# Kernel tuning notes

Measured on AMD Instinct MI355X. Metric: run time of the kernel, lower is better.

Reference implementation:

```python
import jax, jax.numpy as jnp
from jax import lax
import numpy as np

N, L, E, NHEAD, DFF = 16, 1024, 512, 8, 2048
HD = E // NHEAD
NLEVELS = 10  # log2(1024)
S_SCALES = NLEVELS + 1


def setup_inputs() -> dict:
    key = jax.random.key(0)
    ks = jax.random.split(key, 12)
    s = 0.05
    return {
        "src": jax.random.normal(ks[0], (N, L, E), jnp.float32),
        "conv_w": jax.random.normal(ks[1], (NLEVELS, HD, HD, 2), jnp.float32) * s,
        "conv_b": jax.random.normal(ks[2], (NLEVELS, HD), jnp.float32) * s,
        "in_proj_w": jax.random.normal(ks[3], (3 * E, E), jnp.float32) * s,
        "in_proj_b": jax.random.normal(ks[4], (3 * E,), jnp.float32) * s,
        "out_proj_w": jax.random.normal(ks[5], (E, E), jnp.float32) * s,
        "out_proj_b": jax.random.normal(ks[6], (E,), jnp.float32) * s,
        "ln1_w": jnp.ones((E,), jnp.float32),
        "ln1_b": jnp.zeros((E,), jnp.float32),
        "ln2_w": jnp.ones((E,), jnp.float32),
        "ln2_b": jnp.zeros((E,), jnp.float32),
        "w1": jax.random.normal(ks[7], (DFF, E), jnp.float32) * s,
        "b1": jax.random.normal(ks[8], (DFF,), jnp.float32) * s,
        "w2": jax.random.normal(ks[9], (E, DFF), jnp.float32) * s,
        "b2": jax.random.normal(ks[10], (E,), jnp.float32) * s,
    }


def _layer_norm(x, w, b, eps=1e-5):
    mu = jnp.mean(x, axis=-1, keepdims=True)
    var = jnp.mean(jnp.square(x - mu), axis=-1, keepdims=True)
    return (x - mu) * lax.rsqrt(var + eps) * w + b


def _forward(src, conv_w, conv_b, in_proj_w, in_proj_b, out_proj_w, out_proj_b,
             ln1_w, ln1_b, ln2_w, ln2_b, w1, b1, w2, b2):
    n, l, e = src.shape
    hd = e // NHEAD
    # pyramid over 1D spatial dim, channels-first
    out = jnp.transpose(src, (0, 2, 1))  # (N, E, L)
    hidden_vals = [out]
    for i in range(NLEVELS):
        x = out.reshape(n * NHEAD, hd, out.shape[-1])  # (N*H, hd, li)
        x = lax.conv_general_dilated(
            x, conv_w[i], window_strides=(2,), padding='VALID',
            dimension_numbers=('NCH', 'OIH', 'NCH'))
        x = jax.nn.relu(x + conv_b[i][None, :, None])
        out = x.reshape(n, e, x.shape[-1])  # (N, E, li/2)
        # upsample back to full length via repeat_interleave
        hidden_vals.append(jnp.repeat(out, l // out.shape[-1], axis=2))
    hv = jnp.stack(hidden_vals, -1)                      # (N, E, L, S)
    s = hv.shape[-1]
    hv = jnp.transpose(hv, (3, 0, 2, 1)).reshape(s, n * l, e)  # (S, N*L, E)

    # multi-head attention: length-1 query (finest scale) over all scales
    b_ = n * l
    q = hv[0:1] @ in_proj_w[:e].T + in_proj_b[:e]            # (1, B, E)
    k = hv @ in_proj_w[e:2 * e].T + in_proj_b[e:2 * e]       # (S, B, E)
    v = hv @ in_proj_w[2 * e:].T + in_proj_b[2 * e:]         # (S, B, E)
    qh = jnp.transpose(q.reshape(1, b_, NHEAD, hd), (1, 2, 0, 3))  # (B, H, 1, hd)
    kh = jnp.transpose(k.reshape(s, b_, NHEAD, hd), (1, 2, 0, 3))  # (B, H, S, hd)
    vh = jnp.transpose(v.reshape(s, b_, NHEAD, hd), (1, 2, 0, 3))  # (B, H, S, hd)
    scores = jnp.einsum('bhqd,bhkd->bhqk', qh, kh) / jnp.sqrt(jnp.float32(hd))
    attn = jax.nn.softmax(scores, axis=-1)
    o = jnp.einsum('bhqk,bhkd->bhqd', attn, vh)              # (B, H, 1, hd)
    o = o.reshape(b_, e) @ out_proj_w.T + out_proj_b         # (B, E)
    src2 = o.reshape(n, l, e)

    # faithful to source: residual computed then overwritten by norm1(src2)
    x = _layer_norm(src2, ln1_w, ln1_b)
    ff = jax.nn.relu(x @ w1.T + b1) @ w2.T + b2
    return _layer_norm(x + ff, ln2_w, ln2_b)


def reference(src, conv_w, conv_b, in_proj_w, in_proj_b, out_proj_w, out_proj_b,
              ln1_w, ln1_b, ln2_w, ln2_b, w1, b1, w2, b2):
    return _forward(src, conv_w, conv_b, in_proj_w, in_proj_b, out_proj_w,
                    out_proj_b, ln1_w, ln1_b, ln2_w, ln2_b, w1, b1, w2, b2)
```

## Files before the change

### kernel.cpp

```cpp
#include <hip/hip_runtime.h>
#include <hip/hip_bf16.h>
#include <stdint.h>
#include <math.h>

#define NB      16
#define LL      1024
#define EE      512
#define NHEADS  8
#define DFF     2048
#define NLEVELS 10
#define NSCALES 11
#define BROWS   (NB * LL)

typedef unsigned short u16;
typedef __attribute__((ext_vector_type(8))) short bf16x8;
typedef __attribute__((ext_vector_type(4))) float f32x4;

static const size_t B_SRCBF = 0;
static const size_t B_LVLBF = 16777216;
static const size_t B_QKV   = 33538048;
static const size_t B_KVS   = 83869696;
static const size_t B_OBF   = 117391360;
static const size_t B_X     = 134168576;
static const size_t B_XBF   = 167723008;
static const size_t B_WBF   = 184500224;
static const size_t B_FFH   = 0;

__device__ __forceinline__ u16 f2bf(float x) {
    union { float f; uint32_t u; } c; c.f = x;
    uint32_t u = c.u + 0x7FFFu + ((c.u >> 16) & 1u);
    return (u16)(u >> 16);
}
__device__ __forceinline__ float bf2f(u16 v) {
    union { uint32_t u; float f; } c; c.u = ((uint32_t)v) << 16; return c.f;
}
__device__ __forceinline__ void ld8bf(const u16* p, float* f) {
    uint4 r = *(const uint4*)p;
    uint32_t ws[4] = { r.x, r.y, r.z, r.w };
    #pragma unroll
    for (int j = 0; j < 4; j++) {
        union { uint32_t u; float g; } lo, hi;
        lo.u = ws[j] << 16; hi.u = ws[j] & 0xFFFF0000u;
        f[2 * j] = lo.g; f[2 * j + 1] = hi.g;
    }
}
__device__ __forceinline__ void gload16(const u16* g, u16* l) {
    __builtin_amdgcn_global_load_lds(
        (const __attribute__((address_space(1))) void*)g,
        (__attribute__((address_space(3))) void*)l, 16, 0, 0);
}

__global__ void cast_all_kernel(const float* __restrict__ s0, const float* __restrict__ s1,
                                const float* __restrict__ s2, const float* __restrict__ s3,
                                const float* __restrict__ s4, const float* __restrict__ cw,
                                u16* __restrict__ d0, u16* __restrict__ d1,
                                u16* __restrict__ d2, u16* __restrict__ d3,
                                u16* __restrict__ d4, u16* __restrict__ dw)
{
    int bid = blockIdx.x;
    if (bid >= 11264) {
        int base = (bid - 11264) * 1024 + threadIdx.x * 4;
        #pragma unroll
        for (int j = 0; j < 4; j++) {
            int idx = base + j;
            int lvl = idx >> 13, rem = idx & 8191;
            int o = rem >> 7, ck = rem & 127;
            int k = ck >> 6, ci = ck & 63;
            dw[idx] = f2bf(cw[(lvl << 13) + (o << 7) + (ci << 1) + k]);
        }
        return;
    }
    const float* s; u16* d; int nt;
    if      (bid < 8192)  { s = s0; d = d0; nt = 2097152; }
    else if (bid < 8960)  { bid -= 8192;  s = s1; d = d1; nt = 196608; }
    else if (bid < 9216)  { bid -= 8960;  s = s2; d = d2; nt = 65536;  }
    else if (bid < 10240) { bid -= 9216;  s = s3; d = d3; nt = 262144; }
    else                  { bid -= 10240; s = s4; d = d4; nt = 262144; }
    int i = bid * 256 + threadIdx.x;
    if (i < nt) {
        float4 v = ((const float4*)s)[i];
        uint2 o;
        o.x = (uint32_t)f2bf(v.x) | ((uint32_t)f2bf(v.y) << 16);
        o.y = (uint32_t)f2bf(v.z) | ((uint32_t)f2bf(v.w) << 16);
        ((uint2*)d)[i] = o;
    }
}

__global__ __launch_bounds__(256, 2)
void conv_chain_kernel(const u16* __restrict__ src_bf, u16* __restrict__ lvl_bf,
                       const u16* __restrict__ cw, const float* __restrict__ cb)
{
    __shared__ u16 BIG[16384];
    __shared__ u16 MID[8192];
    __shared__ u16 WB[8192];
    const int tid = threadIdx.x;
    const int l = tid & 63, w = tid >> 6;
    const int bid = blockIdx.x;
    const int q  = bid & 3;
    const int h  = (bid >> 2) & 7;
    const int n  = bid >> 5;

    {
        const u16* base = src_bf + ((size_t)n * 1024 + q * 256) * 512 + h * 64;
        #pragma unroll
        for (int j = 0; j < 8; j++) {
            int c = j * 256 + w * 64 + l;
            int row = c >> 3, lch = c & 7;
            int gch = lch ^ (row & 7);
            gload16(base + (size_t)row * 512 + gch * 8,
                    BIG + (size_t)(j * 256 + w * 64) * 8);
        }
    }

    const u16* IN = BIG;
    u16* OUTb = MID;
    int R = 128;
    int T = 512;
    size_t rowOff = 0;
    for (int lvl = 1; lvl <= 8; lvl++) {
        {
            const u16* wsrc = cw + (size_t)(lvl - 1) * 8192;
            #pragma unroll
            for (int j = 0; j < 4; j++) {
                int c = j * 256 + w * 64 + l;
                int o = c >> 4, lch = c & 15;
                int gch = lch ^ (o & 7);
                gload16(wsrc + o * 128 + gch * 8, WB + (size_t)(j * 256 + w * 64) * 8);
            }
        }
        asm volatile("s_waitcnt vmcnt(0)" ::: "memory");
        __syncthreads();

        const int nrt = (R + 15) >> 4;
        const int maxil = 2 * R - 1;
        for (int f = w; f < nrt * 4; f += 4) {
            int rt = f >> 2, nc = f & 3;
            int o = nc * 16 + (l & 15);
            f32x4 acc = {0.f, 0.f, 0.f, 0.f};
            #pragma unroll
            for (int s = 0; s < 4; s++) {
                int il = 2 * (rt * 16 + (l & 15)) + (s >> 1);
                if (il > maxil) il = maxil;
                int ach = (((s & 1) * 4) + (l >> 4)) ^ (il & 7);
                bf16x8 av = *(const bf16x8*)(IN + il * 64 + ach * 8);
                int bch = (s * 4 + (l >> 4)) ^ (o & 7);
                bf16x8 bv = *(const bf16x8*)(WB + o * 128 + bch * 8);
                acc = __builtin_amdgcn_mfma_f32_16x16x32_bf16(av, bv, acc, 0, 0, 0);
            }
            float bb = cb[(lvl - 1) * 64 + o];
            #pragma unroll
            for (int reg = 0; reg < 4; reg++) {
                int rloc = rt * 16 + (l >> 4) * 4 + reg;
                if (rloc < R) {
                    float v = fmaxf(acc[reg] + bb, 0.f);
                    u16 b16 = f2bf(v);
                    lvl_bf[(rowOff + (size_t)n * T + (size_t)q * R + rloc) * 512 + h * 64 + o] = b16;
                    OUTb[rloc * 64 + (((o >> 3) ^ (rloc & 7)) << 3) + (o & 7)] = b16;
                }
            }
        }
        __syncthreads();
        const u16* tmp = IN; IN = OUTb; OUTb = (u16*)tmp;
        rowOff += (size_t)16 * T;
        T >>= 1; R >>= 1;
    }
}

__global__ void conv_tail_kernel(u16* __restrict__ lvl_bf, const u16* __restrict__ cw,
                                 const float* __restrict__ cb)
{
    const int h = blockIdx.x & 7, n = blockIdx.x >> 3;
    const int tid = threadIdx.x;
    __shared__ float L8s[4][64];
    __shared__ float L9s[2][64];
    {
        int r = tid >> 6, c = tid & 63;
        L8s[r][c] = bf2f(lvl_bf[((size_t)16256 + n * 4 + r) * 512 + h * 64 + c]);
    }
    __syncthreads();
    if (tid < 128) {
        int t = tid >> 6, o = tid & 63;
        const u16* wr = cw + (size_t)8 * 8192 + o * 128;
        float acc = cb[8 * 64 + o];
        #pragma unroll
        for (int k = 0; k < 2; k++)
            #pragma unroll 16
            for (int ci = 0; ci < 64; ci++)
                acc += L8s[2 * t + k][ci] * bf2f(wr[k * 64 + ci]);
        acc = fmaxf(acc, 0.f);
        L9s[t][o] = acc;
        lvl_bf[((size_t)16320 + n * 2 + t) * 512 + h * 64 + o] = f2bf(acc);
    }
    __syncthreads();
    if (tid < 64) {
        int o = tid;
        const u16* wr = cw + (size_t)9 * 8192 + o * 128;
        float acc = cb[9 * 64 + o];
        #pragma unroll
        for (int k = 0; k < 2; k++)
            #pragma unroll 16
            for (int ci = 0; ci < 64; ci++)
                acc += L9s[k][ci] * bf2f(wr[k * 64 + ci]);
        acc = fmaxf(acc, 0.f);
        lvl_bf[((size_t)16352 + n) * 512 + h * 64 + o] = f2bf(acc);
    }
}

__global__ __launch_bounds__(512, 4)
void mfma_gemm(const u16* __restrict__ A, const u16* __restrict__ W,
               const float* __restrict__ bias,
               const u16* __restrict__ resb,
               float* __restrict__ Cf, u16* __restrict__ Cb,
               int M, int K, int N, int relu, int gx)
{
    __shared__ u16 lds[36864];
    const int tid = threadIdx.x;
    const int l = tid & 63, w = tid >> 6;
    const int wm = w >> 1, wn = w & 1;

    const int nwg = gridDim.x;
    const int q = nwg >> 3, r = nwg & 7;
    const int xcd = blockIdx.x & 7, idx = blockIdx.x >> 3;
    const int lin = (xcd < r ? xcd * (q + 1) : r * (q + 1) + (xcd - r) * q) + idx;
    const int by = lin / gx, bx = lin - by * gx;
    const int rowBase = by * 256, colBase = bx * 128;

    f32x4 acc[4][4];
    #pragma unroll
    for (int m = 0; m < 4; m++)
        #pragma unroll
        for (int n = 0; n < 4; n++) acc[m][n] = 0.f;

    const u16* gApt[2];
    const u16* gBpt;
    #pragma unroll
    for (int i = 0; i < 2; i++) {
        int G = i * 512 + tid;
        int row = G >> 2, p = G & 3;
        int c = p ^ ((row >> 1) & 3);
        int grow = rowBase + row; if (grow > M - 1) grow = M - 1;
        gApt[i] = A + (size_t)grow * K + c * 8;
    }
    {
        int G = tid;
        int row = G >> 2, p = G & 3;
        int c = p ^ ((row >> 1) & 3);
        gBpt = W + (size_t)(colBase + row) * K + c * 8;
    }

    const int NT = K >> 5;
    auto STAGE = [&](int tt, int buf) {
        const int kb = tt << 5;
        u16* dA = lds + buf * 12288;
        u16* dB = dA + 8192;
        gload16(gApt[0] + kb, dA + (size_t)(w * 64) * 8);
        gload16(gApt[1] + kb, dA + (size_t)(512 + w * 64) * 8);
        gload16(gBpt + kb, dB + (size_t)(w * 64) * 8);
    };
    STAGE(0, 0);
    if (NT > 1) STAGE(1, 1);

    int cbuf = 0, sbuf = 2;
    for (int t = 0; t < NT; ++t) {
        if (t + 1 < NT) asm volatile("s_waitcnt vmcnt(3)" ::: "memory");
        else            asm volatile("s_waitcnt vmcnt(0)" ::: "memory");
        __builtin_amdgcn_s_barrier();
        __builtin_amdgcn_sched_barrier(0);
        if (t + 2 < NT) STAGE(t + 2, sbuf);

        const u16* Ab = lds + cbuf * 12288;
        const u16* Bb = Ab + 8192;
        const int c = l >> 4;
        bf16x8 av[4], bv[4];
        #pragma unroll
        for (int fr = 0; fr < 4; fr++) {
            int row = wm * 64 + fr * 16 + (l & 15);
            av[fr] = *(const bf16x8*)(Ab + row * 32 + ((c ^ ((row >> 1) & 3)) * 8));
        }
        #pragma unroll
        for (int fc = 0; fc < 4; fc++) {
            int col = wn * 64 + fc * 16 + (l & 15);
            bv[fc] = *(const bf16x8*)(Bb + col * 32 + ((c ^ ((col >> 1) & 3)) * 8));
        }
        __builtin_amdgcn_s_setprio(1);
        #pragma unroll
        for (int m = 0; m < 4; m++)
            #pragma unroll
            for (int n = 0; n < 4; n++)
                acc[m][n] = __builtin_amdgcn_mfma_f32_16x16x32_bf16(av[m], bv[n], acc[m][n], 0, 0, 0);
        __builtin_amdgcn_s_setprio(0);

        cbuf = (cbuf == 2) ? 0 : cbuf + 1;
        sbuf = (sbuf == 2) ? 0 : sbuf + 1;
    }
    __builtin_amdgcn_s_barrier();
    __builtin_amdgcn_sched_barrier(0);

    const int cc = colBase + wn * 64 + (l & 15);
    float bs4[4];
    #pragma unroll
    for (int n = 0; n < 4; n++) bs4[n] = bias[cc + n * 16];

    if (Cb) {
        u16* WS = lds + w * 2048;
        #pragma unroll
        for (int hh = 0; hh < 2; hh++) {
            #pragma unroll
            for (int mi = 0; mi < 2; mi++) {
                #pragma unroll
                for (int n = 0; n < 4; n++) {
                    int colv = n * 16 + (l & 15);
                    #pragma unroll
                    for (int reg = 0; reg < 4; reg++) {
                        int rowh = mi * 16 + (l >> 4) * 4 + reg;
                        float v = acc[hh * 2 + mi][n][reg] + bs4[n];
                        if (relu) v = fmaxf(v, 0.f);
                        WS[rowh * 64 + (colv ^ (((rowh >> 2) & 3) << 4))] = f2bf(v);
                    }
                }
            }
            asm volatile("s_waitcnt lgkmcnt(0)" ::: "memory");
            __builtin_amdgcn_sched_barrier(0);
            #pragma unroll
            for (int j = 0; j < 4; j++) {
                int rowh = (l >> 3) + 8 * j;
                int col8 = (l & 7) * 8;
                int colx = col8 ^ (((rowh >> 2) & 3) << 4);
                uint4 v = *(const uint4*)(WS + rowh * 64 + colx);
                int grow = rowBase + wm * 64 + hh * 32 + rowh;
                if (grow < M)
                    *(uint4*)(Cb + (size_t)grow * N + colBase + wn * 64 + col8) = v;
            }
            asm volatile("s_waitcnt lgkmcnt(0)" ::: "memory");
        }
    } else {
        float* WSf = (float*)lds + w * 1024;
        #pragma unroll
        for (int hh = 0; hh < 2; hh++) {
            #pragma unroll
            for (int mi = 0; mi < 2; mi++) {
                #pragma unroll
                for (int n = 0; n < 4; n++) {
                    int colv = n * 16 + (l & 15);
                    #pragma unroll
                    for (int reg = 0; reg < 4; reg++) {
                        int rowh = (l >> 4) * 4 + reg;
                        WSf[rowh * 64 + (colv ^ (((rowh >> 2) & 3) << 4))] =
                            acc[hh * 2 + mi][n][reg] + bs4[n];
                    }
                }
                asm volatile("s_waitcnt lgkmcnt(0)" ::: "memory");
                __builtin_amdgcn_sched_barrier(0);
                #pragma unroll
                for (int j = 0; j < 4; j++) {
                    int rowh = (l >> 4) + 4 * j;
                    int col4 = (l & 15) * 4;
                    int colx = col4 ^ (((rowh >> 2) & 3) << 4);
                    float4 v = *(const float4*)(WSf + rowh * 64 + colx);
                    int grow = rowBase + wm * 64 + hh * 32 + mi * 16 + rowh;
                    if (grow < M) {
                        int gcol = colBase + wn * 64 + col4;
                        if (resb) {
                            uint2 rb = *(const uint2*)&resb[(size_t)grow * N + gcol];
                            v.x += bf2f((u16)(rb.x & 0xFFFF));
                            v.y += bf2f((u16)(rb.x >> 16));
                            v.z += bf2f((u16)(rb.y & 0xFFFF));
                            v.w += bf2f((u16)(rb.y >> 16));
                        }
                        if (relu) {
                            v.x = fmaxf(v.x, 0.f); v.y = fmaxf(v.y, 0.f);
                            v.z = fmaxf(v.z, 0.f); v.w = fmaxf(v.w, 0.f);
                        }
                        *(float4*)&Cf[(size_t)grow * N + gcol] = v;
                    }
                }
                asm volatile("s_waitcnt lgkmcnt(0)" ::: "memory");
            }
        }
    }
}

__global__ void attn_kernel(const u16* __restrict__ QKV, const u16* __restrict__ KVs,
                            u16* __restrict__ O)
{
    const int wv   = threadIdx.x >> 6;
    const int lane = threadIdx.x & 63;
    const int b    = blockIdx.x * 4 + wv;
    const int h    = lane >> 3;
    const int d8   = lane & 7;
    const int n = b >> 10, pos = b & 1023;

    float q[8];
    ld8bf(QKV + (size_t)b * 1536 + h * 64 + d8 * 8, q);

    float sc[NSCALES];
    {
        float kk[8];
        ld8bf(QKV + (size_t)b * 1536 + 512 + h * 64 + d8 * 8, kk);
        float p = 0.f;
        #pragma unroll
        for (int j = 0; j < 8; j++) p += q[j] * kk[j];
        p += __shfl_xor(p, 1); p += __shfl_xor(p, 2); p += __shfl_xor(p, 4);
        sc[0] = p * 0.125f;
    }
    {
        int rowOff = 0;
        #pragma unroll
        for (int s = 1; s <= NLEVELS; s++) {
            int Ls = 1024 >> s;
            int row = rowOff + n * Ls + (pos >> s);
            float kk[8];
            ld8bf(KVs + (size_t)row * 1024 + h * 64 + d8 * 8, kk);
            float p = 0.f;
            #pragma unroll
            for (int j = 0; j < 8; j++) p += q[j] * kk[j];
            p += __shfl_xor(p, 1); p += __shfl_xor(p, 2); p += __shfl_xor(p, 4);
            sc[s] = p * 0.125f;
            rowOff += 16 * Ls;
        }
    }
    float m = sc[0];
    #pragma unroll
    for (int s = 1; s < NSCALES; s++) m = fmaxf(m, sc[s]);
    float sum = 0.f;
    #pragma unroll
    for (int s = 0; s < NSCALES; s++) { sc[s] = __expf(sc[s] - m); sum += sc[s]; }
    float inv = 1.f / sum;

    float o[8] = {};
    {
        float vv[8];
        ld8bf(QKV + (size_t)b * 1536 + 1024 + h * 64 + d8 * 8, vv);
        float a = sc[0] * inv;
        #pragma unroll
        for (int j = 0; j < 8; j++) o[j] += a * vv[j];
    }
    {
        int rowOff = 0;
        #pragma unroll
        for (int s = 1; s <= NLEVELS; s++) {
            int Ls = 1024 >> s;
            int row = rowOff + n * Ls + (pos >> s);
            float vv[8];
            ld8bf(KVs + (size_t)row * 1024 + 512 + h * 64 + d8 * 8, vv);
            float a = sc[s] * inv;
            #pragma unroll
            for (int j = 0; j < 8; j++) o[j] += a * vv[j];
            rowOff += 16 * Ls;
        }
    }
    uint4 pk;
    pk.x = (uint32_t)f2bf(o[0]) | ((uint32_t)f2bf(o[1]) << 16);
    pk.y = (uint32_t)f2bf(o[2]) | ((uint32_t)f2bf(o[3]) << 16);
    pk.z = (uint32_t)f2bf(o[4]) | ((uint32_t)f2bf(o[5]) << 16);
    pk.w = (uint32_t)f2bf(o[6]) | ((uint32_t)f2bf(o[7]) << 16);
    *(uint4*)(O + (size_t)b * 512 + h * 64 + d8 * 8) = pk;
}

__global__ void ln_kernel(const float* __restrict__ in, float* __restrict__ out,
                          const float* __restrict__ w, const float* __restrict__ b,
                          u16* __restrict__ out_bf)
{
    const int l = threadIdx.x & 63;
    const int row = blockIdx.x * 4 + (threadIdx.x >> 6);
    const float* p = in + (size_t)row * EE + l * 8;
    float4 v0 = *(const float4*)p;
    float4 v1 = *(const float4*)(p + 4);
    float s  = v0.x + v0.y + v0.z + v0.w + v1.x + v1.y + v1.z + v1.w;
    float s2 = v0.x * v0.x + v0.y * v0.y + v0.z * v0.z + v0.w * v0.w
             + v1.x * v1.x + v1.y * v1.y + v1.z * v1.z + v1.w * v1.w;
    #pragma unroll
    for (int m = 1; m < 64; m <<= 1) { s += __shfl_xor(s, m); s2 += __shfl_xor(s2, m); }
    float mu  = s * (1.f / 512.f);
    float var = s2 * (1.f / 512.f) - mu * mu;
    float rs  = rsqrtf(var + 1e-5f);
    float4 w0 = *(const float4*)&w[l * 8], w1 = *(const float4*)&w[l * 8 + 4];
    float4 b0 = *(const float4*)&b[l * 8], b1 = *(const float4*)&b[l * 8 + 4];
    float o[8];
    o[0] = (v0.x - mu) * rs * w0.x + b0.x;
    o[1] = (v0.y - mu) * rs * w0.y + b0.y;
    o[2] = (v0.z - mu) * rs * w0.z + b0.z;
    o[3] = (v0.w - mu) * rs * w0.w + b0.w;
    o[4] = (v1.x - mu) * rs * w1.x + b1.x;
    o[5] = (v1.y - mu) * rs * w1.y + b1.y;
    o[6] = (v1.z - mu) * rs * w1.z + b1.z;
    o[7] = (v1.w - mu) * rs * w1.w + b1.w;
    float* po = out + (size_t)row * EE + l * 8;
    *(float4*)po       = make_float4(o[0], o[1], o[2], o[3]);
    *(float4*)(po + 4) = make_float4(o[4], o[5], o[6], o[7]);
    if (out_bf) {
        uint4 pk;
        pk.x = (uint32_t)f2bf(o[0]) | ((uint32_t)f2bf(o[1]) << 16);
        pk.y = (uint32_t)f2bf(o[2]) | ((uint32_t)f2bf(o[3]) << 16);
        pk.z = (uint32_t)f2bf(o[4]) | ((uint32_t)f2bf(o[5]) << 16);
        pk.w = (uint32_t)f2bf(o[6]) | ((uint32_t)f2bf(o[7]) << 16);
        *(uint4*)(out_bf + (size_t)row * EE + l * 8) = pk;
    }
}

extern "C" void kernel_launch(void* const* d_in, const int* in_sizes, int n_in,
                              void* d_out, int out_size, void* d_ws, size_t ws_size,
                              hipStream_t stream)
{
    const float* src        = (const float*)d_in[0];
    const float* conv_w     = (const float*)d_in[1];
    const float* conv_b     = (const float*)d_in[2];
    const float* in_proj_w  = (const float*)d_in[3];
    const float* in_proj_b  = (const float*)d_in[4];
    const float* out_proj_w = (const float*)d_in[5];
    const float* out_proj_b = (const float*)d_in[6];
    const float* ln1_w      = (const float*)d_in[7];
    const float* ln1_b      = (const float*)d_in[8];
    const float* ln2_w      = (const float*)d_in[9];
    const float* ln2_b      = (const float*)d_in[10];
    const float* w1         = (const float*)d_in[11];
    const float* b1         = (const float*)d_in[12];
    const float* w2         = (const float*)d_in[13];
    const float* b2         = (const float*)d_in[14];

    char*  wsb    = (char*)d_ws;
    float* out    = (float*)d_out;
    u16*   src_bf = (u16*)(wsb + B_SRCBF);
    u16*   lvl_bf = (u16*)(wsb + B_LVLBF);
    u16*   QKV    = (u16*)(wsb + B_QKV);
    u16*   KVs    = (u16*)(wsb + B_KVS);
    u16*   O_bf   = (u16*)(wsb + B_OBF);
    float* X      = (float*)(wsb + B_X);
    u16*   X_bf   = (u16*)(wsb + B_XBF);
    u16*   inw_bf = (u16*)(wsb + B_WBF);
    u16*   outw_bf= inw_bf + 786432;
    u16*   w1_bf  = outw_bf + 262144;
    u16*   w2_bf  = w1_bf + 1048576;
    u16*   cw_bf  = w2_bf + 1048576;
    u16*   FFH    = (u16*)(wsb + B_FFH);

    cast_all_kernel<<<11344, 256, 0, stream>>>(src, in_proj_w, out_proj_w, w1, w2, conv_w,
                                               src_bf, inw_bf, outw_bf, w1_bf, w2_bf, cw_bf);

    conv_chain_kernel<<<NB * NHEADS * 4, 256, 0, stream>>>(src_bf, lvl_bf, cw_bf, conv_b);
    conv_tail_kernel<<<NB * NHEADS, 256, 0, stream>>>(lvl_bf, cw_bf, conv_b);

    mfma_gemm<<<64 * 12, 512, 0, stream>>>(
        src_bf, inw_bf, in_proj_b, nullptr, nullptr, QKV, BROWS, EE, 1536, 0, 12);

    mfma_gemm<<<64 * 8, 512, 0, stream>>>(
        lvl_bf, inw_bf + (size_t)512 * 512, in_proj_b + 512, nullptr, nullptr, KVs,
        16368, EE, 1024, 0, 8);

    attn_kernel<<<BROWS / 4, 256, 0, stream>>>(QKV, KVs, O_bf);

    mfma_gemm<<<64 * 4, 512, 0, stream>>>(
        O_bf, outw_bf, out_proj_b, nullptr, X, nullptr, BROWS, EE, EE, 0, 4);

    ln_kernel<<<BROWS / 4, 256, 0, stream>>>(X, X, ln1_w, ln1_b, X_bf);

    mfma_gemm<<<64 * 16, 512, 0, stream>>>(
        X_bf, w1_bf, b1, nullptr, nullptr, FFH, BROWS, EE, DFF, 1, 16);

    mfma_gemm<<<64 * 4, 512, 0, stream>>>(
        FFH, w2_bf, b2, X_bf, out, nullptr, BROWS, DFF, EE, 0, 4);

    ln_kernel<<<BROWS / 4, 256, 0, stream>>>(out, out, ln2_w, ln2_b, nullptr);
}
```

Baseline: 247.0 us.

## Add 256x256-tile double-buffered GEMM for bf16-output projections

Introduces a new GEMM kernel with 256x256 output tiles, BK=64, LDS double buffering with interleaved staging of the next tile across four MFMA sub-phases, and an LDS-staged coalesced bf16 epilogue. It replaces the 256x128 GEMM for the QKV, KV-scale and FFN1 projections to raise arithmetic intensity and cut global traffic per FLOP. It also adds an explicit lgkmcnt wait before the MFMA block in the existing kernel. The larger tile uses 128 KB of LDS and many accumulator registers, which limits occupancy and halves the number of workgroups.

```diff
diff --git a/kernel.cpp b/kernel.cpp
--- a/kernel.cpp
+++ b/kernel.cpp
@@ -282,6 +282,8 @@
             int col = wn * 64 + fc * 16 + (l & 15);
             bv[fc] = *(const bf16x8*)(Bb + col * 32 + ((c ^ ((col >> 1) & 3)) * 8));
         }
+        asm volatile("s_waitcnt lgkmcnt(0)" ::: "memory");
+        __builtin_amdgcn_sched_barrier(0);
         __builtin_amdgcn_s_setprio(1);
         #pragma unroll
         for (int m = 0; m < 4; m++)
@@ -380,6 +382,141 @@
     }
 }
 
+__global__ __launch_bounds__(512, 2)
+void mfma_gemm_big(const u16* __restrict__ A, const u16* __restrict__ W,
+                   const float* __restrict__ bias, u16* __restrict__ Cb,
+                   int M, int K, int N, int relu, int gx)
+{
+    __shared__ u16 lds[65536];
+    const int tid = threadIdx.x;
+    const int l = tid & 63, w = tid >> 6;
+    const int wm = w >> 2, wn = w & 3;
+
+    const int nwg = gridDim.x;
+    const int q = nwg >> 3, r = nwg & 7;
+    const int xcd = blockIdx.x & 7, idx = blockIdx.x >> 3;
+    const int lin = (xcd < r ? xcd * (q + 1) : r * (q + 1) + (xcd - r) * q) + idx;
+    const int by = lin / gx, bx = lin - by * gx;
+    const int rowBase = by * 256, colBase = bx * 256;
+
+    f32x4 acc[8][4];
+    #pragma unroll
+    for (int m = 0; m < 8; m++)
+        #pragma unroll
+        for (int n = 0; n < 4; n++) acc[m][n] = 0.f;
+
+    const u16* gApt[4];
+    const u16* gBpt[4];
+    #pragma unroll
+    for (int j = 0; j < 4; j++) {
+        int G = j * 512 + tid;
+        int row = G >> 3, p = G & 7;
+        int c = p ^ (row & 7);
+        int grow = rowBase + row; if (grow > M - 1) grow = M - 1;
+        gApt[j] = A + (size_t)grow * K + c * 8;
+        gBpt[j] = W + (size_t)(colBase + row) * K + c * 8;
+    }
+
+    const int NT = K >> 6;
+    auto STAGE = [&](int tt, int unit) {
+        const int kb = tt << 6;
+        u16* base = lds + (tt & 1) * 32768;
+        if (unit < 2) {
+            gload16(gApt[unit * 2]     + kb, base + (size_t)((unit * 2)     * 512 + w * 64) * 8);
+            gload16(gApt[unit * 2 + 1] + kb, base + (size_t)((unit * 2 + 1) * 512 + w * 64) * 8);
+        } else {
+            int u = unit - 2;
+            gload16(gBpt[u * 2]     + kb, base + 16384 + (size_t)((u * 2)     * 512 + w * 64) * 8);
+            gload16(gBpt[u * 2 + 1] + kb, base + 16384 + (size_t)((u * 2 + 1) * 512 + w * 64) * 8);
+        }
+    };
+    STAGE(0, 0); STAGE(0, 1); STAGE(0, 2); STAGE(0, 3);
+
+    const int g = l >> 4;
+    for (int t = 0; t < NT; ++t) {
+        asm volatile("s_waitcnt vmcnt(0)" ::: "memory");
+        __builtin_amdgcn_s_barrier();
+        __builtin_amdgcn_sched_barrier(0);
+        const u16* Ab = lds + (t & 1) * 32768;
+        const u16* Bb = Ab + 16384;
+
+        bf16x8 bv[4][2];
+        #pragma unroll
+        for (int p = 0; p < 4; ++p) {
+            bf16x8 av[2][2];
+            #pragma unroll
+            for (int ks = 0; ks < 2; ks++) {
+                #pragma unroll
+                for (int fr = 0; fr < 2; fr++) {
+                    int row = wm * 128 + (p * 2 + fr) * 16 + (l & 15);
+                    av[fr][ks] = *(const bf16x8*)(Ab + row * 64 + (((ks * 4 + g) ^ (row & 7)) * 8));
+                }
+                if (p == 0) {
+                    #pragma unroll
+                    for (int fc = 0; fc < 4; fc++) {
+                        int col = wn * 64 + fc * 16 + (l & 15);
+                        bv[fc][ks] = *(const bf16x8*)(Bb + col * 64 + (((ks * 4 + g) ^ (col & 7)) * 8));
+                    }
+                }
+            }
+            if (t + 1 < NT) STAGE(t + 1, p);
+            asm volatile("s_waitcnt lgkmcnt(0)" ::: "memory");
+            __builtin_amdgcn_sched_barrier(0);
+            __builtin_amdgcn_s_setprio(1);
+            #pragma unroll
+            for (int ks = 0; ks < 2; ks++)
+                #pragma unroll
+                for (int fr = 0; fr < 2; fr++)
+                    #pragma unroll
+                    for (int fc = 0; fc < 4; fc++)
+                        acc[p * 2 + fr][fc] = __builtin_amdgcn_mfma_f32_16x16x32_bf16(
+                            av[fr][ks], bv[fc][ks], acc[p * 2 + fr][fc], 0, 0, 0);
+            __builtin_amdgcn_s_setprio(0);
+            __builtin_amdgcn_sched_barrier(0);
+        }
+    }
+    __builtin_amdgcn_s_barrier();
+    __builtin_amdgcn_sched_barrier(0);
+
+    const int cc = colBase + wn * 64 + (l & 15);
+    float bs4[4];
+    #pragma unroll
+    for (int n = 0; n < 4; n++) bs4[n] = bias[cc + n * 16];
+
+    u16* WS = lds + w * 2048;
+    #pragma unroll
+    for (int grp = 0; grp < 4; grp++) {
+        #pragma unroll
+        for (int mi = 0; mi < 2; mi++) {
+            int mf = grp * 2 + mi;
+            #pragma unroll
+            for (int n = 0; n < 4; n++) {
+                int colv = n * 16 + (l & 15);
+                #pragma unroll
+                for (int reg = 0; reg < 4; reg++) {
+                    int rowh = mi * 16 + (l >> 4) * 4 + reg;
+                    float v = acc[mf][n][reg] + bs4[n];
+                    if (relu) v = fmaxf(v, 0.f);
+                    WS[rowh * 64 + (colv ^ (((rowh >> 2) & 3) << 4))] = f2bf(v);
+                }
+            }
+        }
+        asm volatile("s_waitcnt lgkmcnt(0)" ::: "memory");
+        __builtin_amdgcn_sched_barrier(0);
+        #pragma unroll
+        for (int j = 0; j < 4; j++) {
+            int rowh = (l >> 3) + 8 * j;
+            int col8 = (l & 7) * 8;
+            int colx = col8 ^ (((rowh >> 2) & 3) << 4);
+            uint4 v = *(const uint4*)(WS + rowh * 64 + colx);
+            int grow = rowBase + wm * 128 + grp * 32 + rowh;
+            if (grow < M)
+                *(uint4*)(Cb + (size_t)grow * N + colBase + wn * 64 + col8) = v;
+        }
+        asm volatile("s_waitcnt lgkmcnt(0)" ::: "memory");
+    }
+}
+
 __global__ void attn_kernel(const u16* __restrict__ QKV, const u16* __restrict__ KVs,
                             u16* __restrict__ O)
 {
@@ -540,12 +677,11 @@
     conv_chain_kernel<<<NB * NHEADS * 4, 256, 0, stream>>>(src_bf, lvl_bf, cw_bf, conv_b);
     conv_tail_kernel<<<NB * NHEADS, 256, 0, stream>>>(lvl_bf, cw_bf, conv_b);
 
-    mfma_gemm<<<64 * 12, 512, 0, stream>>>(
-        src_bf, inw_bf, in_proj_b, nullptr, nullptr, QKV, BROWS, EE, 1536, 0, 12);
-
-    mfma_gemm<<<64 * 8, 512, 0, stream>>>(
-        lvl_bf, inw_bf + (size_t)512 * 512, in_proj_b + 512, nullptr, nullptr, KVs,
-        16368, EE, 1024, 0, 8);
+    mfma_gemm_big<<<64 * 6, 512, 0, stream>>>(
+        src_bf, inw_bf, in_proj_b, QKV, BROWS, EE, 1536, 0, 6);
+
+    mfma_gemm_big<<<64 * 4, 512, 0, stream>>>(
+        lvl_bf, inw_bf + (size_t)512 * 512, in_proj_b + 512, KVs, 16368, EE, 1024, 0, 4);
 
     attn_kernel<<<BROWS / 4, 256, 0, stream>>>(QKV, KVs, O_bf);
 
@@ -554,8 +690,8 @@
 
     ln_kernel<<<BROWS / 4, 256, 0, stream>>>(X, X, ln1_w, ln1_b, X_bf);
 
-    mfma_gemm<<<64 * 16, 512, 0, stream>>>(
-        X_bf, w1_bf, b1, nullptr, nullptr, FFH, BROWS, EE, DFF, 1, 16);
+    mfma_gemm_big<<<64 * 8, 512, 0, stream>>>(
+        X_bf, w1_bf, b1, FFH, BROWS, EE, DFF, 1, 8);
 
     mfma_gemm<<<64 * 4, 512, 0, stream>>>(
         FFH, w2_bf, b2, X_bf, out, nullptr, BROWS, DFF, EE, 0, 4);
```

Result: slower. 252.2 us (+2.1%).
